# Kernel optimization log

Measured on AMD Instinct MI355X. Metric: run time of the kernel, lower is better.

The kernel has to match this reference:

```python
import jax, jax.numpy as jnp
import numpy as np

K = 1024          # num_codebook_vectors
D = 256           # latent_dim
BETA = 0.25
DECAY = 0.99
EPS = 1e-5


def setup_inputs() -> dict:
    key = jax.random.key(0)
    k1, k2, k3 = jax.random.split(key, 3)
    return {
        "z": jax.random.normal(k1, (32, 256, 32, 32), dtype=jnp.float32),
        "embedding": jax.random.normal(k2, (K, D), dtype=jnp.float32),
        "ema_cluster_size": jnp.zeros((K,), dtype=jnp.float32),
        "ema_w": jax.random.normal(k3, (K, D), dtype=jnp.float32),
    }


def reference(z, embedding, ema_cluster_size, ema_w):
    # z: [B, C=D, H, W] -> [B, H, W, D]
    zp = jnp.transpose(z, (0, 2, 3, 1))
    zf = zp.reshape(-1, D)                                  # [N, D]

    # pairwise squared distances: ||z||^2 + ||e||^2 - 2 z e^T
    d = (jnp.sum(zf * zf, axis=1, keepdims=True)
         + jnp.sum(embedding * embedding, axis=1)
         - 2.0 * zf @ embedding.T)                           # [N, K]
    idx = jnp.argmin(d, axis=1)                              # [N]

    # one-hot @ embedding == gather
    z_q = jnp.take(embedding, idx, axis=0).reshape(zp.shape)  # [B,H,W,D]

    # EMA codebook update (training path)
    counts = jax.ops.segment_sum(jnp.ones_like(idx, dtype=jnp.float32), idx,
                                 num_segments=K)             # sum of one-hots
    new_cs = ema_cluster_size * DECAY + (1.0 - DECAY) * counts
    n = jnp.sum(new_cs)
    new_cs = (new_cs + EPS) / (n + K * EPS) * n
    dw = jax.ops.segment_sum(zf, idx, num_segments=K)        # encodings^T @ zf
    new_ema_w = ema_w * DECAY + (1.0 - DECAY) * dw
    new_embedding = new_ema_w / new_cs[:, None]

    # commitment loss (z_q computed with OLD embedding, per source order)
    e_latent_loss = jnp.mean((z_q - zp) ** 2)
    loss = BETA * e_latent_loss

    # straight-through (no grad distinction in pure forward)
    z_q_out = jnp.transpose(z_q, (0, 3, 1, 2))               # [B, D, H, W]
    return (z_q_out, idx[:, None], loss, new_embedding, new_cs, new_ema_w)
```

## Files before the change

### kernel.cpp

```cpp
#include <hip/hip_runtime.h>

#define K_CODES 1024
#define D_DIM   256
#define N_VEC   32768
#define BETA    0.25f
#define DECAY   0.99f
#define EPSV    1e-5f

#define OFF_ZQ   0
#define OFF_IDX  8388608
#define OFF_LOSS 8421376
#define OFF_EMB  8421377
#define OFF_CS   8683521
#define OFF_EMAW 8684545

#define WS_EMBT    0
#define WS_ENORM   262144
#define WS_ELOMAX  263168
#define WS_EHIMAX  263169
#define WS_FIXCNT  263170
#define WS_S2      263172
#define WS_ZN2     1311748
#define WS_ZLO2    1344516
#define WS_FIXLIST 1377284
#define WS_OFF     1410052
#define WS_POS     1411076
#define WS_CNT     1412100
#define WS_CHTAB   1413124
#define WS_TC      1415172

#define CHUNK 32
#define DBIAS 512.0f

typedef _Float16 f16;
typedef f16   f16x8 __attribute__((ext_vector_type(8)));
typedef float f32x4 __attribute__((ext_vector_type(4)));

__device__ inline void top2_merge(float& d1, int& j1, float& d2, int& j2,
                                  float od1, int oj1, float od2, int oj2) {
    if (od1 < d1 || (od1 == d1 && oj1 < j1)) {
        float nd2; int nj2;
        if (d1 < od2 || (d1 == od2 && j1 < oj2)) { nd2 = d1; nj2 = j1; }
        else { nd2 = od2; nj2 = oj2; }
        d2 = nd2; j2 = nj2; d1 = od1; j1 = oj1;
    } else {
        if (od1 < d2 || (od1 == d2 && oj1 < j2)) { d2 = od1; j2 = oj1; }
    }
}

__global__ void k_pt(const float* __restrict__ z, const float* __restrict__ emb,
                     float* __restrict__ ws, float* __restrict__ out) {
    if (blockIdx.x == 0 && threadIdx.x == 0) *(int*)(ws + WS_FIXCNT) = 0;
    if (blockIdx.x < 256) {
        int j    = blockIdx.x * 4 + (threadIdx.x >> 6);
        int lane = threadIdx.x & 63;
        float4 v = reinterpret_cast<const float4*>(emb + j * D_DIM)[lane];
        ws[(lane * 4 + 0) * 1024 + j] = v.x;
        ws[(lane * 4 + 1) * 1024 + j] = v.y;
        ws[(lane * 4 + 2) * 1024 + j] = v.z;
        ws[(lane * 4 + 3) * 1024 + j] = v.w;
        float s = v.x * v.x + v.y * v.y + v.z * v.z + v.w * v.w;
        float hx = (float)(f16)v.x, hy = (float)(f16)v.y;
        float hz = (float)(f16)v.z, hw = (float)(f16)v.w;
        float lx = v.x - hx, ly = v.y - hy, lz = v.z - hz, lw = v.w - hw;
        float sl = lx * lx + ly * ly + lz * lz + lw * lw;
        float sh = hx * hx + hy * hy + hz * hz + hw * hw;
        #pragma unroll
        for (int o = 32; o > 0; o >>= 1) {
            s  += __shfl_xor(s,  o, 64);
            sl += __shfl_xor(sl, o, 64);
            sh += __shfl_xor(sh, o, 64);
        }
        if (lane == 0) {
            ws[WS_ENORM + j] = s;
            atomicMax((int*)(ws + WS_ELOMAX), __float_as_int(sqrtf(sl)));
            atomicMax((int*)(ws + WS_EHIMAX), __float_as_int(sqrtf(sh)));
        }
    } else if (blockIdx.x < 384) {
        int slot = (blockIdx.x - 256) * 256 + threadIdx.x;
        int lane = slot & 63;
        int kbjt = slot >> 6;
        int kb   = kbjt & 7;
        int jt   = kbjt >> 3;
        int j    = jt * 16 + (lane & 15);
        int d0   = kb * 32 + (lane >> 4) * 8;
        float4 e0 = *reinterpret_cast<const float4*>(emb + j * D_DIM + d0);
        float4 e1 = *reinterpret_cast<const float4*>(emb + j * D_DIM + d0 + 4);
        f16x8 w;
        w[0] = (f16)e0.x; w[1] = (f16)e0.y; w[2] = (f16)e0.z; w[3] = (f16)e0.w;
        w[4] = (f16)e1.x; w[5] = (f16)e1.y; w[6] = (f16)e1.z; w[7] = (f16)e1.w;
        f16* dst = (f16*)(out + OFF_EMAW + 3);
        *reinterpret_cast<f16x8*>(dst + slot * 8) = w;
    } else {
        __shared__ float tile[32][257];
        const int bid = blockIdx.x - 384;
        const int n0  = bid * 32;
        const int b   = n0 >> 10;
        const int hw0 = n0 & 1023;
        const int tid = threadIdx.x;
        #pragma unroll 8
        for (int rep = 0; rep < 32; ++rep) {
            int elem = rep * 256 + tid;
            int d = elem >> 5, hwl = elem & 31;
            tile[hwl][d] = z[b * (D_DIM * 1024) + d * 1024 + hw0 + hwl];
        }
        __syncthreads();
        #pragma unroll 8
        for (int row = 0; row < 32; ++row)
            out[OFF_ZQ + (long)(n0 + row) * 256 + tid] = tile[row][tid];
        if (tid < 32) {
            float sn = 0.f, sl = 0.f;
            for (int d = 0; d < 256; ++d) {
                float v  = tile[tid][d];
                float lo = v - (float)(f16)v;
                sn += v * v; sl += lo * lo;
            }
            ws[WS_ZN2  + n0 + tid] = sn;
            ws[WS_ZLO2 + n0 + tid] = sl;
        }
    }
}

__global__ __launch_bounds__(256, 2)
void k_main(float* __restrict__ out, float* __restrict__ ws) {
    __shared__ float els_s[512];

    const int tid  = threadIdx.x;
    const int lane = tid & 63;
    const int w    = tid >> 6;
    const int bid  = blockIdx.x;
    const int rt   = bid >> 1;
    const int jh   = bid & 1;
    const int n0   = rt * 64;
    const float* zf = out + OFF_ZQ;
    const f16* Bw = (const f16*)(out + OFF_EMAW + 3);

    if (bid == 0) {
        #pragma unroll
        for (int r = 0; r < 4; ++r) out[OFF_CS + r * 256 + tid] = 0.f;
        if (tid == 0) out[OFF_LOSS] = 0.f;
    }
    els_s[tid]       = ws[WS_ENORM + jh * 512 + tid] + DBIAS;
    els_s[tid + 256] = ws[WS_ENORM + jh * 512 + tid + 256] + DBIAS;

    const int aoff = (lane >> 4) * 8;
    const int c    = lane & 15;
    const long arow = n0 + w * 16 + c;
    f16x8 a0, a1, a2, a3, a4, a5, a6, a7;
#define LOADA(KB, AV) { \
    float4 p0 = *reinterpret_cast<const float4*>(zf + arow * 256 + KB * 32 + aoff); \
    float4 p1 = *reinterpret_cast<const float4*>(zf + arow * 256 + KB * 32 + aoff + 4); \
    AV = (f16x8){(f16)p0.x, (f16)p0.y, (f16)p0.z, (f16)p0.w, \
                 (f16)p1.x, (f16)p1.y, (f16)p1.z, (f16)p1.w}; }
    LOADA(0, a0) LOADA(1, a1) LOADA(2, a2) LOADA(3, a3)
    LOADA(4, a4) LOADA(5, a5) LOADA(6, a6) LOADA(7, a7)
#undef LOADA
    __syncthreads();

    unsigned k1_0 = 0xFFFFFFFFu, k2_0 = 0xFFFFFFFFu;
    unsigned k1_1 = 0xFFFFFFFFu, k2_1 = 0xFFFFFFFFu;
    unsigned k1_2 = 0xFFFFFFFFu, k2_2 = 0xFFFFFFFFu;
    unsigned k1_3 = 0xFFFFFFFFu, k2_3 = 0xFFFFFFFFu;

    for (int pass = 0; pass < 16; ++pass) {
        const int jt0 = jh * 32 + pass * 2;
        const f16* B0 = Bw + ((size_t)jt0 * 8 * 64 + lane) * 8;
        f32x4 acc0 = (f32x4){0.f, 0.f, 0.f, 0.f};
        f32x4 acc1 = (f32x4){0.f, 0.f, 0.f, 0.f};
#define KBSTEP(KB, AV) { \
        f16x8 b0 = *reinterpret_cast<const f16x8*>(B0 + (size_t)KB * 512); \
        f16x8 b1 = *reinterpret_cast<const f16x8*>(B0 + (size_t)(KB + 8) * 512); \
        acc0 = __builtin_amdgcn_mfma_f32_16x16x32_f16(AV, b0, acc0, 0, 0, 0); \
        acc1 = __builtin_amdgcn_mfma_f32_16x16x32_f16(AV, b1, acc1, 0, 0, 0); }
        KBSTEP(0, a0) KBSTEP(1, a1) KBSTEP(2, a2) KBSTEP(3, a3)
        KBSTEP(4, a4) KBSTEP(5, a5) KBSTEP(6, a6) KBSTEP(7, a7)
#undef KBSTEP
        const int jl0 = pass * 32 + c;
        const float en0 = els_s[jl0];
        const float en1 = els_s[jl0 + 16];
        const unsigned jg0 = (unsigned)(jh * 512 + jl0);
#define FOLD(EN, ACC, JJ, R) { \
        float _d = fmaf(-2.f, (ACC), (EN)); \
        unsigned _k = (__float_as_uint(_d) & 0xFFFFFC00u) | (JJ); \
        unsigned _mx = max(k1_##R, _k); \
        k1_##R = min(k1_##R, _k); \
        k2_##R = min(k2_##R, _mx); }
        FOLD(en0, acc0[0], jg0,       0) FOLD(en1, acc1[0], jg0 + 16u, 0)
        FOLD(en0, acc0[1], jg0,       1) FOLD(en1, acc1[1], jg0 + 16u, 1)
        FOLD(en0, acc0[2], jg0,       2) FOLD(en1, acc1[2], jg0 + 16u, 2)
        FOLD(en0, acc0[3], jg0,       3) FOLD(en1, acc1[3], jg0 + 16u, 3)
#undef FOLD
    }

#define MERGE(R, RIDX) { \
        unsigned K1 = k1_##R, K2 = k2_##R; \
        _Pragma("unroll") \
        for (int s = 1; s < 16; s <<= 1) { \
            unsigned o1 = (unsigned)__shfl_xor((int)K1, s, 64); \
            unsigned o2 = (unsigned)__shfl_xor((int)K2, s, 64); \
            unsigned mx = max(K1, o1); \
            K1 = min(K1, o1); \
            K2 = min(min(K2, o2), mx); \
        } \
        if (c == 0) { \
            int row = n0 + w * 16 + (lane >> 4) * 4 + RIDX; \
            *reinterpret_cast<float2*>(ws + WS_S2 + ((size_t)row * 2 + jh) * 2) = \
                (float2){__uint_as_float(K1), __uint_as_float(K2)}; } }
    MERGE(0, 0) MERGE(1, 1) MERGE(2, 2) MERGE(3, 3)
#undef MERGE
}

__global__ void k_merge(float* __restrict__ ws, float* __restrict__ out) {
    int n = blockIdx.x * 256 + threadIdx.x;
    const float2* S2 = reinterpret_cast<const float2*>(ws + WS_S2) + (size_t)n * 2;
    float2 ea = S2[0], eb = S2[1];
    unsigned k1a = __float_as_uint(ea.x), k2a = __float_as_uint(ea.y);
    unsigned k1b = __float_as_uint(eb.x), k2b = __float_as_uint(eb.y);
    unsigned mx = max(k1a, k1b);
    unsigned k1 = min(k1a, k1b);
    unsigned k2 = min(min(k2a, k2b), mx);
    int j1 = (int)(k1 & 0x3FFu);
    float d1 = __uint_as_float(k1 & 0xFFFFFC00u) - DBIAS;
    float d2 = __uint_as_float(k2 & 0xFFFFFC00u) - DBIAS;
    out[OFF_IDX + n] = (float)j1;
    float zn2 = ws[WS_ZN2 + n];
    float margin = 4.f * (sqrtf(ws[WS_ZLO2 + n]) * ws[WS_EHIMAX] +
                          sqrtf(zn2) * ws[WS_ELOMAX]) + 0.05f
                 + 0.4f;
    if (d2 - d1 <= margin) {
        int p = atomicAdd((int*)(ws + WS_FIXCNT), 1);
        ((int*)(ws + WS_FIXLIST))[p] = n;
    } else {
        atomicAdd(out + OFF_CS + j1, 1.0f);
        atomicAdd(out + OFF_LOSS, d1 + zn2);
    }
    #pragma unroll
    for (int r = 0; r < 2; ++r)
        *reinterpret_cast<float4*>(out + OFF_EMAW + ((size_t)n * 2 + r) * 4) =
            (float4){0.f, 0.f, 0.f, 0.f};
}

__global__ void k_fix(const float* __restrict__ ws_c, float* __restrict__ out) {
    __shared__ float zr[8][256];
    __shared__ float rd[8][4]; __shared__ int rj[8][4];
    const int tid = threadIdx.x;
    const int cnt = *(const int*)(ws_c + WS_FIXCNT);
    const int* fixlist = (const int*)(ws_c + WS_FIXLIST);
    const int groups = (cnt + 7) >> 3;
    const float4 en = *reinterpret_cast<const float4*>(ws_c + WS_ENORM + tid * 4);

    for (int g = blockIdx.x; g < groups; g += gridDim.x) {
        int nrow[8];
        #pragma unroll
        for (int r = 0; r < 8; ++r) {
            int slot = g * 8 + r;
            nrow[r] = (slot < cnt) ? fixlist[slot] : -1;
        }
        #pragma unroll
        for (int r = 0; r < 8; ++r)
            zr[r][tid] = (nrow[r] >= 0) ? out[OFF_ZQ + (long)nrow[r] * 256 + tid] : 0.f;
        __syncthreads();

        float acc[8][4];
        #pragma unroll
        for (int r = 0; r < 8; ++r)
            #pragma unroll
            for (int q = 0; q < 4; ++q) acc[r][q] = 0.f;
        #pragma unroll 4
        for (int d = 0; d < 256; ++d) {
            float4 e = *reinterpret_cast<const float4*>(ws_c + WS_EMBT + d * 1024 + tid * 4);
            #pragma unroll
            for (int r = 0; r < 8; ++r) {
                float zd = zr[r][d];
                acc[r][0] += zd * e.x; acc[r][1] += zd * e.y;
                acc[r][2] += zd * e.z; acc[r][3] += zd * e.w;
            }
        }
        #pragma unroll
        for (int r = 0; r < 8; ++r) {
            float best = 3.4e38f; int bj = 0;
            #pragma unroll
            for (int q = 0; q < 4; ++q) {
                int j = tid * 4 + q;
                float v = ((const float*)&en)[q] - 2.f * acc[r][q];
                if (v < best || (v == best && j < bj)) { best = v; bj = j; }
            }
            #pragma unroll
            for (int o = 1; o < 64; o <<= 1) {
                float ov = __shfl_xor(best, o, 64);
                int   oj = __shfl_xor(bj, o, 64);
                if (ov < best || (ov == best && oj < bj)) { best = ov; bj = oj; }
            }
            if ((tid & 63) == 0) { rd[r][tid >> 6] = best; rj[r][tid >> 6] = bj; }
        }
        __syncthreads();
        if (tid < 8) {
            int r = tid;
            float v = rd[r][0]; int j = rj[r][0];
            #pragma unroll
            for (int ww = 1; ww < 4; ++ww)
                if (rd[r][ww] < v || (rd[r][ww] == v && rj[r][ww] < j)) { v = rd[r][ww]; j = rj[r][ww]; }
            int slot = g * 8 + r;
            if (slot < cnt) {
                int n = fixlist[slot];
                out[OFF_IDX + n] = (float)j;
                atomicAdd(out + OFF_CS + j, 1.0f);
                atomicAdd(out + OFF_LOSS, v + ws_c[WS_ZN2 + n]);
            }
        }
        __syncthreads();
    }
}

__global__ void k_scan(const float* __restrict__ ema_cs, float* __restrict__ ws,
                       float* __restrict__ out) {
    __shared__ float s[K_CODES];
    int tid = threadIdx.x;
    float cntf = out[OFF_CS + tid];
    int   cnt  = (int)cntf;
    float raw  = ema_cs[tid] * DECAY + 0.01f * cntf;

    s[tid] = cntf;
    __syncthreads();
    for (int off = 1; off < 1024; off <<= 1) {
        float v = (tid >= off) ? s[tid - off] : 0.f;
        __syncthreads();
        s[tid] += v;
        __syncthreads();
    }
    int excl = (int)(s[tid] - cntf);
    ((int*)(ws + WS_OFF))[tid] = excl;
    ((int*)(ws + WS_POS))[tid] = excl;
    ((int*)(ws + WS_CNT))[tid] = cnt;
    __syncthreads();

    int nch = (cnt + CHUNK - 1) / CHUNK;
    s[tid] = (float)nch;
    __syncthreads();
    for (int off = 1; off < 1024; off <<= 1) {
        float v = (tid >= off) ? s[tid - off] : 0.f;
        __syncthreads();
        s[tid] += v;
        __syncthreads();
    }
    int chexcl = (int)s[tid] - nch;
    int* chtab = (int*)(ws + WS_CHTAB);
    for (int k = 0; k < nch; ++k)
        chtab[chexcl + k] = (tid << 16) | k;
    if (tid == 1023) *(int*)(ws + WS_TC) = chexcl + nch;
    __syncthreads();

    s[tid] = raw;
    __syncthreads();
    for (int st = 512; st > 0; st >>= 1) {
        if (tid < st) s[tid] += s[tid + st];
        __syncthreads();
    }
    float ntot = s[0];
    out[OFF_CS + tid] = (raw + EPSV) / (ntot + K_CODES * EPSV) * ntot;
    if (tid == 0)
        out[OFF_LOSS] = out[OFF_LOSS] * (BETA / (float)(N_VEC * D_DIM));
}

__global__ void k_scatter(const float* __restrict__ out_c, float* __restrict__ ws) {
    int n = blockIdx.x * 256 + threadIdx.x;
    int j = (int)out_c[OFF_IDX + n];
    int p = atomicAdd((int*)(ws + WS_POS) + j, 1);
    ((int*)(ws + WS_FIXLIST))[p] = n;
}

__global__ void k_dw2(const float* __restrict__ ws, float* __restrict__ out) {
    __shared__ int midx[CHUNK];
    const int b = blockIdx.x;
    if (b >= *(const int*)(ws + WS_TC)) return;
    const int tab = ((const int*)(ws + WS_CHTAB))[b];
    const int j   = tab >> 16;
    const int lc  = tab & 0xffff;
    const int off = ((const int*)(ws + WS_OFF))[j];
    const int cnt = ((const int*)(ws + WS_CNT))[j];
    const int base = lc * CHUNK;
    const int m    = min(CHUNK, cnt - base);
    const int tid  = threadIdx.x;
    if (tid < CHUNK)
        midx[tid] = (tid < m) ? ((const int*)(ws + WS_FIXLIST))[off + base + tid] : 0;
    __syncthreads();
    float acc = 0.f;
    for (int i = 0; i < m; ++i)
        acc += out[OFF_ZQ + (long)midx[i] * 256 + tid];
    atomicAdd(out + OFF_EMAW + j * 256 + tid, acc);
}

__global__ void k_tail(const float* __restrict__ emb, const float* __restrict__ ema_w,
                       float* __restrict__ out) {
    const int tid = threadIdx.x;
    if (blockIdx.x < 256) {
        int i4 = blockIdx.x * 256 + tid;
        int j  = i4 >> 6;
        float4 dw = *reinterpret_cast<float4*>(out + OFF_EMAW + i4 * 4);
        float4 ew = *reinterpret_cast<const float4*>(ema_w + i4 * 4);
        float inv = 1.f / out[OFF_CS + j];
        float4 nw = {ew.x * DECAY + 0.01f * dw.x, ew.y * DECAY + 0.01f * dw.y,
                     ew.z * DECAY + 0.01f * dw.z, ew.w * DECAY + 0.01f * dw.w};
        *reinterpret_cast<float4*>(out + OFF_EMAW + i4 * 4) = nw;
        float4 nb = {nw.x * inv, nw.y * inv, nw.z * inv, nw.w * inv};
        *reinterpret_cast<float4*>(out + OFF_EMB + i4 * 4) = nb;
    } else {
        __shared__ float erows[32][257];
        __shared__ int js[32];
        const int n0  = (blockIdx.x - 256) * 32;
        const int b   = n0 >> 10;
        const int hw0 = n0 & 1023;
        if (tid < 32) js[tid] = (int)out[OFF_IDX + n0 + tid];
        __syncthreads();
        #pragma unroll 4
        for (int r = 0; r < 32; ++r)
            erows[r][tid] = emb[js[r] * D_DIM + tid];
        __syncthreads();
        const long zqb = (long)b * (D_DIM * 1024) + hw0;
        #pragma unroll 4
        for (int rep = 0; rep < 32; ++rep) {
            int elem = rep * 256 + tid;
            int d    = elem >> 5;
            int nl   = elem & 31;
            out[OFF_ZQ + zqb + d * 1024 + nl] = erows[nl][d];
        }
    }
}

extern "C" void kernel_launch(void* const* d_in, const int* in_sizes, int n_in,
                              void* d_out, int out_size, void* d_ws, size_t ws_size,
                              hipStream_t stream) {
    const float* z      = (const float*)d_in[0];
    const float* emb    = (const float*)d_in[1];
    const float* ema_cs = (const float*)d_in[2];
    const float* ema_w  = (const float*)d_in[3];
    float* out = (float*)d_out;
    float* ws  = (float*)d_ws;

    hipLaunchKernelGGL(k_pt,      dim3(1408), dim3(256),  0, stream, z, emb, ws, out);
    hipLaunchKernelGGL(k_main,    dim3(1024), dim3(256),  0, stream, out, ws);
    hipLaunchKernelGGL(k_merge,   dim3(128),  dim3(256),  0, stream, ws, out);
    hipLaunchKernelGGL(k_fix,     dim3(512),  dim3(256),  0, stream, ws, out);
    hipLaunchKernelGGL(k_scan,    dim3(1),    dim3(1024), 0, stream, ema_cs, ws, out);
    hipLaunchKernelGGL(k_scatter, dim3(128),  dim3(256),  0, stream, out, ws);
    hipLaunchKernelGGL(k_dw2,     dim3(2048), dim3(256),  0, stream, ws, out);
    hipLaunchKernelGGL(k_tail,    dim3(1280), dim3(256),  0, stream, emb, ema_w, out);
}
```

Baseline: 189.8 us.

## Split codebook search into quarters with XCD-aware block mapping

The distance/argmin kernel now splits the 1024 codes into four quarters instead of two, doubling the grid to 2048 blocks. Each block's partial top-2 is written into a 4-way slot per row, and the merge kernel folds four partials instead of two. Blocks are remapped so that all four quarter-blocks of a row tile share the same XCD, so the repeated z-row reads can hit that die's L2. The cost is that each row tile's A operand is loaded and converted to f16 four times instead of twice, plus a slightly larger partial-result buffer.

Result: slower. 207.4 us (+9.3%).

```diff
diff --git a/kernel.cpp b/kernel.cpp
--- a/kernel.cpp
+++ b/kernel.cpp
@@ -35,18 +35,6 @@
 typedef _Float16 f16;
 typedef f16   f16x8 __attribute__((ext_vector_type(8)));
 typedef float f32x4 __attribute__((ext_vector_type(4)));
-
-__device__ inline void top2_merge(float& d1, int& j1, float& d2, int& j2,
-                                  float od1, int oj1, float od2, int oj2) {
-    if (od1 < d1 || (od1 == d1 && oj1 < j1)) {
-        float nd2; int nj2;
-        if (d1 < od2 || (d1 == od2 && j1 < oj2)) { nd2 = d1; nj2 = j1; }
-        else { nd2 = od2; nj2 = oj2; }
-        d2 = nd2; j2 = nj2; d1 = od1; j1 = oj1;
-    } else {
-        if (od1 < d2 || (od1 == d2 && oj1 < j2)) { d2 = od1; j2 = oj1; }
-    }
-}
 
 __global__ void k_pt(const float* __restrict__ z, const float* __restrict__ emb,
                      float* __restrict__ ws, float* __restrict__ out) {
@@ -123,25 +111,26 @@
 
 __global__ __launch_bounds__(256, 2)
 void k_main(float* __restrict__ out, float* __restrict__ ws) {
-    __shared__ float els_s[512];
+    __shared__ float els_s[256];
 
     const int tid  = threadIdx.x;
     const int lane = tid & 63;
     const int w    = tid >> 6;
-    const int bid  = blockIdx.x;
-    const int rt   = bid >> 1;
-    const int jh   = bid & 1;
+    const int orig = blockIdx.x;
+    const int xcd  = orig & 7;
+    const int lid  = orig >> 3;
+    const int rt   = xcd * 64 + (lid >> 2);
+    const int jq   = lid & 3;
     const int n0   = rt * 64;
     const float* zf = out + OFF_ZQ;
     const f16* Bw = (const f16*)(out + OFF_EMAW + 3);
 
-    if (bid == 0) {
+    if (orig == 0) {
         #pragma unroll
         for (int r = 0; r < 4; ++r) out[OFF_CS + r * 256 + tid] = 0.f;
         if (tid == 0) out[OFF_LOSS] = 0.f;
     }
-    els_s[tid]       = ws[WS_ENORM + jh * 512 + tid] + DBIAS;
-    els_s[tid + 256] = ws[WS_ENORM + jh * 512 + tid + 256] + DBIAS;
+    els_s[tid] = ws[WS_ENORM + jq * 256 + tid] + DBIAS;
 
     const int aoff = (lane >> 4) * 8;
     const int c    = lane & 15;
@@ -162,8 +151,8 @@
     unsigned k1_2 = 0xFFFFFFFFu, k2_2 = 0xFFFFFFFFu;
     unsigned k1_3 = 0xFFFFFFFFu, k2_3 = 0xFFFFFFFFu;
 
-    for (int pass = 0; pass < 16; ++pass) {
-        const int jt0 = jh * 32 + pass * 2;
+    for (int pass = 0; pass < 8; ++pass) {
+        const int jt0 = jq * 16 + pass * 2;
         const f16* B0 = Bw + ((size_t)jt0 * 8 * 64 + lane) * 8;
         f32x4 acc0 = (f32x4){0.f, 0.f, 0.f, 0.f};
         f32x4 acc1 = (f32x4){0.f, 0.f, 0.f, 0.f};
@@ -178,7 +167,7 @@
         const int jl0 = pass * 32 + c;
         const float en0 = els_s[jl0];
         const float en1 = els_s[jl0 + 16];
-        const unsigned jg0 = (unsigned)(jh * 512 + jl0);
+        const unsigned jg0 = (unsigned)(jq * 256 + jl0);
 #define FOLD(EN, ACC, JJ, R) { \
         float _d = fmaf(-2.f, (ACC), (EN)); \
         unsigned _k = (__float_as_uint(_d) & 0xFFFFFC00u) | (JJ); \
@@ -204,7 +193,7 @@
         } \
         if (c == 0) { \
             int row = n0 + w * 16 + (lane >> 4) * 4 + RIDX; \
-            *reinterpret_cast<float2*>(ws + WS_S2 + ((size_t)row * 2 + jh) * 2) = \
+            *reinterpret_cast<float2*>(ws + WS_S2 + ((size_t)row * 4 + jq) * 2) = \
                 (float2){__uint_as_float(K1), __uint_as_float(K2)}; } }
     MERGE(0, 0) MERGE(1, 1) MERGE(2, 2) MERGE(3, 3)
 #undef MERGE
@@ -212,13 +201,16 @@
 
 __global__ void k_merge(float* __restrict__ ws, float* __restrict__ out) {
     int n = blockIdx.x * 256 + threadIdx.x;
-    const float2* S2 = reinterpret_cast<const float2*>(ws + WS_S2) + (size_t)n * 2;
-    float2 ea = S2[0], eb = S2[1];
-    unsigned k1a = __float_as_uint(ea.x), k2a = __float_as_uint(ea.y);
-    unsigned k1b = __float_as_uint(eb.x), k2b = __float_as_uint(eb.y);
-    unsigned mx = max(k1a, k1b);
-    unsigned k1 = min(k1a, k1b);
-    unsigned k2 = min(min(k2a, k2b), mx);
+    const float2* S2 = reinterpret_cast<const float2*>(ws + WS_S2) + (size_t)n * 4;
+    float2 ea = S2[0], eb = S2[1], ec = S2[2], ed = S2[3];
+    unsigned k1 = __float_as_uint(ea.x), k2 = __float_as_uint(ea.y);
+    unsigned o1, mx;
+    o1 = __float_as_uint(eb.x); mx = max(k1, o1); k1 = min(k1, o1);
+    k2 = min(min(k2, __float_as_uint(eb.y)), mx);
+    o1 = __float_as_uint(ec.x); mx = max(k1, o1); k1 = min(k1, o1);
+    k2 = min(min(k2, __float_as_uint(ec.y)), mx);
+    o1 = __float_as_uint(ed.x); mx = max(k1, o1); k1 = min(k1, o1);
+    k2 = min(min(k2, __float_as_uint(ed.y)), mx);
     int j1 = (int)(k1 & 0x3FFu);
     float d1 = __uint_as_float(k1 & 0xFFFFFC00u) - DBIAS;
     float d2 = __uint_as_float(k2 & 0xFFFFFC00u) - DBIAS;
@@ -438,7 +430,7 @@
     float* ws  = (float*)d_ws;
 
     hipLaunchKernelGGL(k_pt,      dim3(1408), dim3(256),  0, stream, z, emb, ws, out);
-    hipLaunchKernelGGL(k_main,    dim3(1024), dim3(256),  0, stream, out, ws);
+    hipLaunchKernelGGL(k_main,    dim3(2048), dim3(256),  0, stream, out, ws);
     hipLaunchKernelGGL(k_merge,   dim3(128),  dim3(256),  0, stream, ws, out);
     hipLaunchKernelGGL(k_fix,     dim3(512),  dim3(256),  0, stream, ws, out);
     hipLaunchKernelGGL(k_scan,    dim3(1),    dim3(1024), 0, stream, ema_cs, ws, out);
```
